# Performance work log

Measured on AMD Instinct MI355X. Metric: run time of the kernel, lower is better.

## Reference

```python
import jax, jax.numpy as jnp
import numpy as np

C_IN = 128   # pair channel dim
H = 4        # heads
DH = 32      # per-head dim (c_hidden // no_heads = 128 // 4)
R = 96       # low-rank bias rank (hard-coded self.Rank)
N = 384      # sequence length (pair rep is N x N)
S_DIM = 449  # s_inputs feature dim (c_in + 449 into bias MLPs)
MLP_H = 256  # bias MLP hidden width
EPS = 1e-5


def setup_inputs() -> dict:
    key = jax.random.key(0)
    ks = jax.random.split(key, 16)
    w = lambda k, shp, s=0.02: (jax.random.normal(k, shp) * s).astype(jnp.float32)
    return {
        "x": jax.random.normal(ks[0], (N, N, C_IN), dtype=jnp.float32),
        "s_inputs": jax.random.normal(ks[1], (N, S_DIM), dtype=jnp.float32),
        "ln_gamma": jnp.ones((C_IN,), jnp.float32),
        "ln_beta": jnp.zeros((C_IN,), jnp.float32),
        # q flashbias MLP (Linear->Tanh->Linear->Tanh->Linear, no bias)
        "Wq1": w(ks[2], (C_IN + S_DIM, MLP_H)),
        "Wq2": w(ks[3], (MLP_H, MLP_H)),
        "Wq3": w(ks[4], (MLP_H, H * R)),
        # k flashbias MLP
        "Wk1": w(ks[5], (C_IN + S_DIM, MLP_H)),
        "Wk2": w(ks[6], (MLP_H, MLP_H)),
        "Wk3": w(ks[7], (MLP_H, H * R)),
        # OpenFold-style gated Attention params
        "Wq_att": w(ks[8], (C_IN, H * DH)),
        "Wk_att": w(ks[9], (C_IN, H * DH)),
        "Wv_att": w(ks[10], (C_IN, H * DH)),
        "Wg": w(ks[11], (C_IN, H * DH)),
        "bg": jnp.zeros((H * DH,), jnp.float32),
        "Wo": w(ks[12], (H * DH, C_IN)),
        "bo": jnp.zeros((C_IN,), jnp.float32),
        "id": 10,  # id < 16 -> low-rank flashbias path
    }


def _layer_norm(x, gamma, beta):
    mu = jnp.mean(x, axis=-1, keepdims=True)
    var = jnp.var(x, axis=-1, keepdims=True)
    return (x - mu) * jax.lax.rsqrt(var + EPS) * gamma + beta


def _bias_mlp(z, W1, W2, W3):
    # [N, C+449] -> [N, H*R] -> [1, H, N, R]
    h = jnp.tanh(jnp.tanh(z @ W1) @ W2) @ W3
    return jnp.transpose(h.reshape(N, H, R), (1, 0, 2))[None]


def reference(x, s_inputs, ln_gamma, ln_beta, Wq1, Wq2, Wq3, Wk1, Wk2, Wk3,
              Wq_att, Wk_att, Wv_att, Wg, bg, Wo, bo, id=10):
    # starting=True, eval mode, s_inputs given, id < 16 -> low-rank bias path
    x = _layer_norm(x, ln_gamma, ln_beta)                       # [N, N, C]

    # low-rank triangle-bias factors (shared across rows, broadcast over dim 0)
    q_bias = _bias_mlp(jnp.concatenate([x.mean(1), s_inputs], -1), Wq1, Wq2, Wq3)  # [1,H,N,R]
    k_bias = _bias_mlp(jnp.concatenate([x.mean(0), s_inputs], -1), Wk1, Wk2, Wk3)  # [1,H,N,R]

    # multi-head attention over the last sequence axis, per row
    def heads(z, W):  # [N, N, C] -> [N, H, N, DH]
        return jnp.transpose((z @ W).reshape(N, N, H, DH), (0, 2, 1, 3))

    q = heads(x, Wq_att) * (1.0 / np.sqrt(DH)).astype(np.float32)
    k = heads(x, Wk_att)
    v = heads(x, Wv_att)

    scores = jnp.einsum("ihqd,ihkd->ihqk", q, k)                # [N,H,N,N]
    scores = scores + jnp.einsum("bhqr,bhkr->bhqk", q_bias, k_bias)  # broadcast over rows
    a = jax.nn.softmax(scores, axis=-1)

    o = jnp.einsum("ihqk,ihkd->ihqd", a, v)                     # [N,H,N,DH]
    o = jnp.transpose(o, (0, 2, 1, 3)).reshape(N, N, H * DH)
    g = jax.nn.sigmoid(x @ Wg + bg)                              # gating
    out = (g * o) @ Wo + bo                                      # [N, N, C]
    return out
```

## Files before the change

### kernel.cpp

```cpp
#include <hip/hip_runtime.h>
#include <cstdint>
#include <cstddef>

typedef _Float16 f16;
typedef __attribute__((ext_vector_type(2))) _Float16 f16x2;
typedef __attribute__((ext_vector_type(4))) _Float16 f16x4;
typedef __attribute__((ext_vector_type(8))) _Float16 f16x8;
typedef __attribute__((ext_vector_type(4))) float f32x4;

#define MFMA_16x16x32(a,b,c) __builtin_amdgcn_mfma_f32_16x16x32_f16((a),(b),(c),0,0,0)
#define MFMA_16x16x16(a,b,c) __builtin_amdgcn_mfma_f32_16x16x16f16((a),(b),(c),0,0,0)

#define NSEQ 384
#define CIN 128
#define NH 4
#define DHD 32
#define RNK 96
#define SDIM 449
#define MHID 256
#define NN (NSEQ*NSEQ)
#define LOG2E 1.4426950408889634f

#define KPAD 608
#define ZSTR 616
#define HSTR 264
#define OFF_W1 0
#define SZ_W1 (MHID*KPAD)
#define OFF_W2 (2*SZ_W1)
#define SZ_W2 (MHID*MHID)
#define OFF_W3 (OFF_W2 + 2*SZ_W2)
#define SZ_W3 ((NH*RNK)*MHID)
#define WMLP_TOT (OFF_W3 + 2*SZ_W3)

__global__ __launch_bounds__(256) void k_convert(const float* __restrict__ Wq, const float* __restrict__ Wk,
    const float* __restrict__ Wv, const float* __restrict__ Wg, const float* __restrict__ Wo,
    f16* __restrict__ W4T, f16* __restrict__ WoT) {
  int idx = blockIdx.x*256 + threadIdx.x;
  int c = idx >> 7, kk = idx & 127;
  if (c < 512) {
    int mat = c >> 7, cc = c & 127;
    const float* src = mat==0 ? Wq : (mat==1 ? Wk : (mat==2 ? Wv : Wg));
    W4T[c*CIN + kk] = (f16)src[kk*CIN + cc];
  } else {
    int cc = c - 512;
    WoT[cc*CIN + kk] = (f16)Wo[kk*CIN + cc];
  }
}

__global__ __launch_bounds__(256) void k_convert2(const float* __restrict__ Wq1, const float* __restrict__ Wq2,
    const float* __restrict__ Wq3, const float* __restrict__ Wk1, const float* __restrict__ Wk2,
    const float* __restrict__ Wk3, f16* __restrict__ wmlp) {
  int idx = blockIdx.x*256 + threadIdx.x;
  float val;
  if (idx < OFF_W2) {
    int m = idx / SZ_W1, r = idx - m*SZ_W1;
    int c = r / KPAD, kk = r - c*KPAD;
    const float* src = m ? Wk1 : Wq1;
    val = (kk < SDIM + CIN) ? src[kk*MHID + c] : 0.f;
  } else if (idx < OFF_W3) {
    int r = idx - OFF_W2;
    int m = r >> 16, rr = r & 65535;
    int c = rr >> 8, kk = rr & 255;
    const float* src = m ? Wk2 : Wq2;
    val = src[kk*MHID + c];
  } else {
    int r = idx - OFF_W3;
    int m = r / SZ_W3, rr = r - m*SZ_W3;
    int c = rr >> 8, kk = rr & 255;
    const float* src = m ? Wk3 : Wq3;
    val = src[kk*(NH*RNK) + c];
  }
  wmlp[idx] = (f16)val;
}

__global__ __launch_bounds__(256) void k_ln(const float* __restrict__ x, const float* __restrict__ gamma,
    const float* __restrict__ beta, f16* __restrict__ xn, float* __restrict__ rowm) {
  int b = blockIdx.x;
  int i = b >> 2, jbase = (b & 3) * 96;
  int t = threadIdx.x, wave = t >> 6, lane = t & 63;
  int half = lane >> 5, l31 = lane & 31;
  int c0 = l31 * 4;
  __shared__ float racc[CIN];
  if (t < CIN) racc[t] = 0.f;
  float4 g4 = *(const float4*)&gamma[c0];
  float4 b4 = *(const float4*)&beta[c0];
  float a0=0,a1=0,a2=0,a3=0;
  __syncthreads();
  for (int it = 0; it < 12; ++it) {
    int j = jbase + it*8 + wave*2 + half;
    const float4 v = *(const float4*)&x[(size_t)(i*NSEQ + j)*CIN + c0];
    float s = (v.x+v.y)+(v.z+v.w);
    float ss = (v.x*v.x+v.y*v.y)+(v.z*v.z+v.w*v.w);
#pragma unroll
    for (int off = 16; off >= 1; off >>= 1) { s += __shfl_xor(s, off); ss += __shfl_xor(ss, off); }
    float mean = s * (1.0f/CIN);
    float var = ss * (1.0f/CIN) - mean*mean;
    float rs = rsqrtf(var + 1e-5f);
    float y0 = (v.x-mean)*rs*g4.x + b4.x;
    float y1 = (v.y-mean)*rs*g4.y + b4.y;
    float y2 = (v.z-mean)*rs*g4.z + b4.z;
    float y3 = (v.w-mean)*rs*g4.w + b4.w;
    f16x4 w; w[0]=(f16)y0; w[1]=(f16)y1; w[2]=(f16)y2; w[3]=(f16)y3;
    *(f16x4*)&xn[(size_t)(i*NSEQ + j)*CIN + c0] = w;
    a0+=y0; a1+=y1; a2+=y2; a3+=y3;
  }
  atomicAdd(&racc[c0], a0); atomicAdd(&racc[c0+1], a1);
  atomicAdd(&racc[c0+2], a2); atomicAdd(&racc[c0+3], a3);
  __syncthreads();
  if (t < CIN) atomicAdd(&rowm[i*CIN + t], racc[t] * (1.0f/NSEQ));
}

__global__ __launch_bounds__(256) void k_colmean(const f16* __restrict__ xn, float* __restrict__ colm) {
  int j = blockIdx.x; int t = threadIdx.x;
  int c = t & 127, half = t >> 7;
  float acc = 0.f;
  int i0 = half*192;
#pragma unroll 4
  for (int ii = i0; ii < i0 + 192; ++ii)
    acc += (float)xn[(size_t)(ii*NSEQ + j)*CIN + c];
  __shared__ float sb[256];
  sb[t] = acc;
  __syncthreads();
  if (t < 128) colm[j*CIN + t] = (sb[t] + sb[t+128]) * (1.0f/NSEQ);
}

__global__ __launch_bounds__(256) void k_mlp2(const float* __restrict__ rowm, const float* __restrict__ colm,
    const float* __restrict__ sinp, const f16* __restrict__ wmlp,
    float* __restrict__ qbT, float* __restrict__ kbT) {
  int b = blockIdx.x;
  bool isQ = b < 12;
  int r0 = (isQ ? b : b - 12) * 32;
  const float* mean = isQ ? rowm : colm;
  const f16* W1T = wmlp + (isQ ? 0 : SZ_W1);
  const f16* W2T = wmlp + OFF_W2 + (isQ ? 0 : SZ_W2);
  const f16* W3T = wmlp + OFF_W3 + (isQ ? 0 : SZ_W3);
  float* outp = isQ ? qbT : kbT;
  int t = threadIdx.x, wave = t >> 6, lane = t & 63;
  int l15 = lane & 15, quad = lane >> 4;
  int rt = wave & 1, ch = wave >> 1;

  __shared__ __align__(16) f16 z[32*ZSTR];
  __shared__ __align__(16) f16 hbuf[2][32*HSTR];

  for (int idx = t; idx < 32*KPAD; idx += 256) {
    int row = idx / KPAD, u = idx - row*KPAD;
    float v;
    if (u < CIN) v = mean[(r0+row)*CIN + u];
    else if (u < CIN + SDIM) v = sinp[(r0+row)*SDIM + (u - CIN)];
    else v = 0.f;
    z[row*ZSTR + u] = (f16)v;
  }
  __syncthreads();

  {
    f32x4 acc[8];
#pragma unroll
    for (int c = 0; c < 8; ++c) acc[c] = (f32x4){0,0,0,0};
    for (int ks = 0; ks < 19; ++ks) {
      f16x8 af = *(const f16x8*)&z[(rt*16 + l15)*ZSTR + ks*32 + quad*8];
#pragma unroll
      for (int c = 0; c < 8; ++c) {
        f16x8 bf = *(const f16x8*)&W1T[(size_t)((ch*8 + c)*16 + l15)*KPAD + ks*32 + quad*8];
        acc[c] = MFMA_16x16x32(af, bf, acc[c]);
      }
    }
#pragma unroll
    for (int c = 0; c < 8; ++c) {
      int col = (ch*8 + c)*16 + l15;
#pragma unroll
      for (int r = 0; r < 4; ++r) {
        float th = 1.f - 2.f/(1.f + __expf(2.f*acc[c][r]));
        hbuf[0][(rt*16 + quad*4 + r)*HSTR + col] = (f16)th;
      }
    }
  }
  __syncthreads();

  {
    f32x4 acc[8];
#pragma unroll
    for (int c = 0; c < 8; ++c) acc[c] = (f32x4){0,0,0,0};
    for (int ks = 0; ks < 8; ++ks) {
      f16x8 af = *(const f16x8*)&hbuf[0][(rt*16 + l15)*HSTR + ks*32 + quad*8];
#pragma unroll
      for (int c = 0; c < 8; ++c) {
        f16x8 bf = *(const f16x8*)&W2T[(size_t)((ch*8 + c)*16 + l15)*MHID + ks*32 + quad*8];
        acc[c] = MFMA_16x16x32(af, bf, acc[c]);
      }
    }
#pragma unroll
    for (int c = 0; c < 8; ++c) {
      int col = (ch*8 + c)*16 + l15;
#pragma unroll
      for (int r = 0; r < 4; ++r) {
        float th = 1.f - 2.f/(1.f + __expf(2.f*acc[c][r]));
        hbuf[1][(rt*16 + quad*4 + r)*HSTR + col] = (f16)th;
      }
    }
  }
  __syncthreads();

  {
    f32x4 acc[12];
#pragma unroll
    for (int c = 0; c < 12; ++c) acc[c] = (f32x4){0,0,0,0};
    for (int ks = 0; ks < 8; ++ks) {
      f16x8 af = *(const f16x8*)&hbuf[1][(rt*16 + l15)*HSTR + ks*32 + quad*8];
#pragma unroll
      for (int c = 0; c < 12; ++c) {
        f16x8 bf = *(const f16x8*)&W3T[(size_t)((ch*12 + c)*16 + l15)*MHID + ks*32 + quad*8];
        acc[c] = MFMA_16x16x32(af, bf, acc[c]);
      }
    }
#pragma unroll
    for (int c = 0; c < 12; ++c) {
      int o = (ch*12 + c)*16 + l15;
#pragma unroll
      for (int r = 0; r < 4; ++r)
        outp[o*NSEQ + r0 + rt*16 + quad*4 + r] = acc[c][r];
    }
  }
}

__global__ __launch_bounds__(128) void k_bias(const float* __restrict__ qbT, const float* __restrict__ kbT,
    float* __restrict__ bias4) {
  int b = blockIdx.x;
  int h = b / 96, kg = b - h*96;
  int t = threadIdx.x;
  __shared__ float4 kr[RNK];
  if (t < RNK) kr[t] = *(const float4*)&kbT[(size_t)(h*RNK + t)*NSEQ + kg*4];
  __syncthreads();
  float acc[3][4];
#pragma unroll
  for (int m = 0; m < 3; ++m)
#pragma unroll
    for (int r = 0; r < 4; ++r) acc[m][r] = 0.f;
  for (int r = 0; r < RNK; ++r) {
    float4 kv = kr[r];
    const float* qrow = qbT + (size_t)(h*RNK + r)*NSEQ;
    float q0 = qrow[t], q1 = qrow[t+128], q2 = qrow[t+256];
    acc[0][0]+=q0*kv.x; acc[0][1]+=q0*kv.y; acc[0][2]+=q0*kv.z; acc[0][3]+=q0*kv.w;
    acc[1][0]+=q1*kv.x; acc[1][1]+=q1*kv.y; acc[1][2]+=q1*kv.z; acc[1][3]+=q1*kv.w;
    acc[2][0]+=q2*kv.x; acc[2][1]+=q2*kv.y; acc[2][2]+=q2*kv.z; acc[2][3]+=q2*kv.w;
  }
#pragma unroll
  for (int m = 0; m < 3; ++m) {
    int q = t + m*128;
    f32x4 w; w[0]=acc[m][0]*LOG2E; w[1]=acc[m][1]*LOG2E; w[2]=acc[m][2]*LOG2E; w[3]=acc[m][3]*LOG2E;
    *(f32x4*)&bias4[((size_t)b*NSEQ + q)*4] = w;
  }
}

__global__ __launch_bounds__(256) void k_proj(const f16* __restrict__ xn, const f16* __restrict__ W4T,
    const float* __restrict__ bg, f16* __restrict__ qb, f16* __restrict__ kb, f16* __restrict__ vb,
    f16* __restrict__ gb) {
  int mb = blockIdx.x;
  int t = threadIdx.x, wave = t >> 6, lane = t & 63;
  int l15 = lane & 15, quad = lane >> 4;
  int m0 = wave*32;
  __shared__ __align__(16) f16 Bs[128*128];
  size_t grow = (size_t)mb*128 + m0;
  f16x8 af[2][4];
#pragma unroll
  for (int mt = 0; mt < 2; ++mt)
#pragma unroll
    for (int kt = 0; kt < 4; ++kt)
      af[mt][kt] = *(const f16x8*)&xn[(grow + mt*16 + l15)*CIN + (kt*4 + quad)*8];
  int i = mb/3, j0 = (mb - (mb/3)*3)*128 + m0;
  for (int nb = 0; nb < 4; ++nb) {
    for (int p = 0; p < 8; ++p) {
      int c = p*256 + t; int row = c >> 4, ci = c & 15;
      int sw = (ci ^ (row & 15)) * 8;
      *(f16x8*)&Bs[row*128 + sw] = *(const f16x8*)&W4T[(size_t)(nb*128 + row)*CIN + ci*8];
    }
    __syncthreads();
#pragma unroll
    for (int ct = 0; ct < 8; ++ct) {
      f32x4 acc0 = (f32x4){0,0,0,0}, acc1 = (f32x4){0,0,0,0};
#pragma unroll
      for (int kt = 0; kt < 4; ++kt) {
        f16x8 bf = *(const f16x8*)&Bs[(ct*16 + l15)*128 + ((kt*4 + quad) ^ l15)*8];
        acc0 = MFMA_16x16x32(af[0][kt], bf, acc0);
        acc1 = MFMA_16x16x32(af[1][kt], bf, acc1);
      }
      int col = nb*128 + ct*16 + l15;
      int cc = col & 127;
      int hh = cc >> 5, d = cc & 31;
      if (nb == 3) {
        float bgv = bg[cc];
#pragma unroll
        for (int mt = 0; mt < 2; ++mt) {
          f32x4 a = mt ? acc1 : acc0;
#pragma unroll
          for (int r = 0; r < 4; ++r) {
            int jj = j0 + mt*16 + quad*4 + r;
            float sg = 1.0f/(1.0f + __expf(-(a[r] + bgv)));
            gb[(size_t)(i*NSEQ + jj)*CIN + cc] = (f16)sg;
          }
        }
      } else if (nb == 2) {
#pragma unroll
        for (int mt = 0; mt < 2; ++mt) {
          f32x4 a = mt ? acc1 : acc0;
#pragma unroll
          for (int r = 0; r < 4; ++r) {
            int jj = j0 + mt*16 + quad*4 + r;
            vb[((size_t)(i*NH + hh)*DHD + d)*NSEQ + jj] = (f16)a[r];
          }
        }
      } else {
        f16* dstb = nb==0 ? qb : kb;
        float scale = nb==0 ? 0.25503576722f : 1.0f;
#pragma unroll
        for (int mt = 0; mt < 2; ++mt) {
          f32x4 a = mt ? acc1 : acc0;
#pragma unroll
          for (int r = 0; r < 4; ++r) {
            int jj = j0 + mt*16 + quad*4 + r;
            dstb[((size_t)(i*NH + hh)*NSEQ + jj)*DHD + d] = (f16)(a[r]*scale);
          }
        }
      }
    }
    __syncthreads();
  }
}

__global__ __launch_bounds__(256, 4) void k_attn(const f16* __restrict__ qg, const f16* __restrict__ kg,
    const f16* __restrict__ vg, const float* __restrict__ bias4, f16* __restrict__ og) {
  int b = blockIdx.x; int h = b / NSEQ; int i = b - h*NSEQ;
  int t = threadIdx.x; int wave = t >> 6; int lane = t & 63;
  int l15 = lane & 15, quad = lane >> 4;
  size_t base = (size_t)(i*NH + h) * NSEQ * DHD;
  int qt0 = wave*6;
  f16x8 qf[6];
#pragma unroll
  for (int s = 0; s < 6; ++s)
    qf[s] = *(const f16x8*)&qg[base + (size_t)((qt0+s)*16 + l15)*DHD + quad*8];
  f32x4 oa[6][2];
  float lsum[6];
#pragma unroll
  for (int s = 0; s < 6; ++s) { lsum[s] = 0.f; oa[s][0] = (f32x4){0,0,0,0}; oa[s][1] = (f32x4){0,0,0,0}; }
  const f16* kp  = kg + base + (size_t)l15*DHD + quad*8;
  const f16* vt  = vg + base;
  const f16* vp0 = vt + (size_t)l15*NSEQ + quad*4;
  const f16* vp1 = vt + (size_t)(l15+16)*NSEQ + quad*4;
  const float* bp = bias4 + (((size_t)h*96 + quad)*NSEQ + qt0*16 + l15)*4;
  for (int kt = 0; kt < 24; ++kt) {
    f16x8 kf = *(const f16x8*)kp;
    f16x4 vf0 = *(const f16x4*)(vp0 + kt*16);
    f16x4 vf1 = *(const f16x4*)(vp1 + kt*16);
    f32x4 cb[6];
#pragma unroll
    for (int s = 0; s < 6; ++s) cb[s] = *(const f32x4*)(bp + s*64);
    kp += 16*DHD; bp += 4*NSEQ*4;
#pragma unroll
    for (int s = 0; s < 6; ++s) {
      f32x4 st = MFMA_16x16x32(kf, qf[s], cb[s]);
      float p0 = __builtin_amdgcn_exp2f(st[0]);
      float p1 = __builtin_amdgcn_exp2f(st[1]);
      float p2 = __builtin_amdgcn_exp2f(st[2]);
      float p3 = __builtin_amdgcn_exp2f(st[3]);
      lsum[s] += (p0 + p1) + (p2 + p3);
      f16x4 pa; pa[0]=(f16)p0; pa[1]=(f16)p1; pa[2]=(f16)p2; pa[3]=(f16)p3;
      oa[s][0] = MFMA_16x16x16(pa, vf0, oa[s][0]);
      oa[s][1] = MFMA_16x16x16(pa, vf1, oa[s][1]);
    }
  }
#pragma unroll
  for (int s = 0; s < 6; ++s) {
    float lf = lsum[s];
    lf += __shfl_xor(lf, 16);
    lf += __shfl_xor(lf, 32);
    float inv = 1.0f / lf;
#pragma unroll
    for (int r = 0; r < 4; ++r) {
      float invr = __shfl(inv, quad*4 + r);
      int qrow = (qt0+s)*16 + quad*4 + r;
      size_t ob = (size_t)(i*NSEQ + qrow)*(NH*DHD) + h*DHD;
      og[ob + l15]      = (f16)(oa[s][0][r] * invr);
      og[ob + 16 + l15] = (f16)(oa[s][1][r] * invr);
    }
  }
}

__global__ __launch_bounds__(256) void k_final(const f16* __restrict__ gb, const f16* __restrict__ ob,
    const f16* __restrict__ WoT, const float* __restrict__ bo, float* __restrict__ out) {
  int mb = blockIdx.x;
  int t = threadIdx.x, wave = t >> 6, lane = t & 63;
  int l15 = lane & 15, quad = lane >> 4;
  __shared__ __align__(16) f16 Bs[128*128];
  for (int p = 0; p < 8; ++p) {
    int c = p*256 + t; int row = c >> 4, ci = c & 15;
    int sw = (ci ^ (row & 15)) * 8;
    *(f16x8*)&Bs[row*128 + sw] = *(const f16x8*)&WoT[row*CIN + ci*8];
  }
  int m0 = wave*32;
  size_t grow = (size_t)mb*128 + m0;
  f16x8 af[2][4];
#pragma unroll
  for (int mt = 0; mt < 2; ++mt)
#pragma unroll
    for (int kt = 0; kt < 4; ++kt) {
      size_t off = (grow + mt*16 + l15)*CIN + (kt*4 + quad)*8;
      f16x8 gv = *(const f16x8*)&gb[off];
      f16x8 ov = *(const f16x8*)&ob[off];
      af[mt][kt] = gv*ov;
    }
  __syncthreads();
#pragma unroll
  for (int ct = 0; ct < 8; ++ct) {
    f32x4 acc0 = (f32x4){0,0,0,0}, acc1 = (f32x4){0,0,0,0};
#pragma unroll
    for (int kt = 0; kt < 4; ++kt) {
      f16x8 bf = *(const f16x8*)&Bs[(ct*16 + l15)*128 + ((kt*4 + quad) ^ l15)*8];
      acc0 = MFMA_16x16x32(af[0][kt], bf, acc0);
      acc1 = MFMA_16x16x32(af[1][kt], bf, acc1);
    }
    float bov = bo[ct*16 + l15];
#pragma unroll
    for (int mt = 0; mt < 2; ++mt) {
      f32x4 a = mt ? acc1 : acc0;
#pragma unroll
      for (int r = 0; r < 4; ++r) {
        int mrow = (int)(grow) + mt*16 + quad*4 + r;
        out[(size_t)mrow*CIN + ct*16 + l15] = a[r] + bov;
      }
    }
  }
}

extern "C" void kernel_launch(void* const* d_in, const int* in_sizes, int n_in,
                              void* d_out, int out_size, void* d_ws, size_t ws_size,
                              hipStream_t stream) {
  (void)in_sizes; (void)n_in; (void)out_size; (void)ws_size;
  const float* x    = (const float*)d_in[0];
  const float* sinp = (const float*)d_in[1];
  const float* gam  = (const float*)d_in[2];
  const float* bet  = (const float*)d_in[3];
  const float* Wq1  = (const float*)d_in[4];
  const float* Wq2  = (const float*)d_in[5];
  const float* Wq3  = (const float*)d_in[6];
  const float* Wk1  = (const float*)d_in[7];
  const float* Wk2  = (const float*)d_in[8];
  const float* Wk3  = (const float*)d_in[9];
  const float* Wqa  = (const float*)d_in[10];
  const float* Wka  = (const float*)d_in[11];
  const float* Wva  = (const float*)d_in[12];
  const float* Wg   = (const float*)d_in[13];
  const float* bg   = (const float*)d_in[14];
  const float* Wo   = (const float*)d_in[15];
  const float* bo   = (const float*)d_in[16];
  float* out = (float*)d_out;

  char* w = (char*)d_ws;
  auto carve = [&](size_t bytes) { char* p = w; w += (bytes + 255) & ~(size_t)255; return p; };
  f16*   xn    = (f16*)carve((size_t)NN*CIN*2);
  f16*   qb    = (f16*)carve((size_t)NN*CIN*2);
  f16*   kb    = (f16*)carve((size_t)NN*CIN*2);
  f16*   vb    = (f16*)carve((size_t)NN*CIN*2);
  f16*   gbuf  = (f16*)carve((size_t)NN*CIN*2);
  float* bias4 = (float*)carve((size_t)NH*NSEQ*NSEQ*4);
  float* rowm  = (float*)carve((size_t)NSEQ*CIN*4);
  float* colm  = (float*)carve((size_t)NSEQ*CIN*4);
  float* qbT   = (float*)carve((size_t)(NH*RNK)*NSEQ*4);
  float* kbT   = (float*)carve((size_t)(NH*RNK)*NSEQ*4);
  f16*   W4T   = (f16*)carve((size_t)512*CIN*2);
  f16*   WoT   = (f16*)carve((size_t)CIN*CIN*2);
  f16*   wmlp  = (f16*)carve((size_t)WMLP_TOT*2);
  f16*   obuf  = xn;

  hipMemsetAsync(rowm, 0, (size_t)NSEQ*CIN*4, stream);
  k_convert<<<320, 256, 0, stream>>>(Wqa, Wka, Wva, Wg, Wo, W4T, WoT);
  k_convert2<<<WMLP_TOT/256, 256, 0, stream>>>(Wq1, Wq2, Wq3, Wk1, Wk2, Wk3, wmlp);
  k_ln<<<NSEQ*4, 256, 0, stream>>>(x, gam, bet, xn, rowm);
  k_colmean<<<NSEQ, 256, 0, stream>>>(xn, colm);
  k_mlp2<<<24, 256, 0, stream>>>(rowm, colm, sinp, wmlp, qbT, kbT);
  k_bias<<<NH*96, 128, 0, stream>>>(qbT, kbT, bias4);
  k_proj<<<1152, 256, 0, stream>>>(xn, W4T, bg, qb, kb, vb, gbuf);
  k_attn<<<NH*NSEQ, 256, 0, stream>>>(qb, kb, vb, bias4, obuf);
  k_final<<<1152, 256, 0, stream>>>(gbuf, obuf, WoT, bo, out);
}
```

Before: 446.9 us.

## Fold low-rank bias into attention QK via extra MFMAs, drop bias kernel

Removes the k_bias kernel and its materialized 4xNxN fp32 bias tensor. The attention kernel instead computes the bias on the fly as extra rank-96 MFMA k-steps, using fp16 q/k bias factors written directly by the MLP kernel (LOG2E folded into the q factor). V is now stored in the same row-major layout as Q/K and gathered with strided scalar loads. Occupancy hint drops from 4 to 2 blocks per CU because of the extra register fragments. Bias precision drops from fp32 to fp16 inputs.

```diff
diff --git a/kernel.cpp b/kernel.cpp
--- a/kernel.cpp
+++ b/kernel.cpp
@@ -126,7 +126,7 @@
 
 __global__ __launch_bounds__(256) void k_mlp2(const float* __restrict__ rowm, const float* __restrict__ colm,
     const float* __restrict__ sinp, const f16* __restrict__ wmlp,
-    float* __restrict__ qbT, float* __restrict__ kbT) {
+    f16* __restrict__ qb2, f16* __restrict__ kb2) {
   int b = blockIdx.x;
   bool isQ = b < 12;
   int r0 = (isQ ? b : b - 12) * 32;
@@ -134,7 +134,8 @@
   const f16* W1T = wmlp + (isQ ? 0 : SZ_W1);
   const f16* W2T = wmlp + OFF_W2 + (isQ ? 0 : SZ_W2);
   const f16* W3T = wmlp + OFF_W3 + (isQ ? 0 : SZ_W3);
-  float* outp = isQ ? qbT : kbT;
+  f16* dst = isQ ? qb2 : kb2;
+  float oscale = isQ ? LOG2E : 1.0f;
   int t = threadIdx.x, wave = t >> 6, lane = t & 63;
   int l15 = lane & 15, quad = lane >> 4;
   int rt = wave & 1, ch = wave >> 1;
@@ -214,40 +215,15 @@
     }
 #pragma unroll
     for (int c = 0; c < 12; ++c) {
-      int o = (ch*12 + c)*16 + l15;
-#pragma unroll
-      for (int r = 0; r < 4; ++r)
-        outp[o*NSEQ + r0 + rt*16 + quad*4 + r] = acc[c][r];
-    }
-  }
-}
-
-__global__ __launch_bounds__(128) void k_bias(const float* __restrict__ qbT, const float* __restrict__ kbT,
-    float* __restrict__ bias4) {
-  int b = blockIdx.x;
-  int h = b / 96, kg = b - h*96;
-  int t = threadIdx.x;
-  __shared__ float4 kr[RNK];
-  if (t < RNK) kr[t] = *(const float4*)&kbT[(size_t)(h*RNK + t)*NSEQ + kg*4];
-  __syncthreads();
-  float acc[3][4];
-#pragma unroll
-  for (int m = 0; m < 3; ++m)
-#pragma unroll
-    for (int r = 0; r < 4; ++r) acc[m][r] = 0.f;
-  for (int r = 0; r < RNK; ++r) {
-    float4 kv = kr[r];
-    const float* qrow = qbT + (size_t)(h*RNK + r)*NSEQ;
-    float q0 = qrow[t], q1 = qrow[t+128], q2 = qrow[t+256];
-    acc[0][0]+=q0*kv.x; acc[0][1]+=q0*kv.y; acc[0][2]+=q0*kv.z; acc[0][3]+=q0*kv.w;
-    acc[1][0]+=q1*kv.x; acc[1][1]+=q1*kv.y; acc[1][2]+=q1*kv.z; acc[1][3]+=q1*kv.w;
-    acc[2][0]+=q2*kv.x; acc[2][1]+=q2*kv.y; acc[2][2]+=q2*kv.z; acc[2][3]+=q2*kv.w;
-  }
-#pragma unroll
-  for (int m = 0; m < 3; ++m) {
-    int q = t + m*128;
-    f32x4 w; w[0]=acc[m][0]*LOG2E; w[1]=acc[m][1]*LOG2E; w[2]=acc[m][2]*LOG2E; w[3]=acc[m][3]*LOG2E;
-    *(f32x4*)&bias4[((size_t)b*NSEQ + q)*4] = w;
+      int T = ch*12 + c;
+      int hh = T / 6;
+      int rr = (T - hh*6)*16 + l15;
+#pragma unroll
+      for (int r = 0; r < 4; ++r) {
+        int q = r0 + rt*16 + quad*4 + r;
+        dst[((size_t)hh*NSEQ + q)*RNK + rr] = (f16)(acc[c][r] * oscale);
+      }
+    }
   }
 }
 
@@ -298,18 +274,8 @@
             gb[(size_t)(i*NSEQ + jj)*CIN + cc] = (f16)sg;
           }
         }
-      } else if (nb == 2) {
-#pragma unroll
-        for (int mt = 0; mt < 2; ++mt) {
-          f32x4 a = mt ? acc1 : acc0;
-#pragma unroll
-          for (int r = 0; r < 4; ++r) {
-            int jj = j0 + mt*16 + quad*4 + r;
-            vb[((size_t)(i*NH + hh)*DHD + d)*NSEQ + jj] = (f16)a[r];
-          }
-        }
       } else {
-        f16* dstb = nb==0 ? qb : kb;
+        f16* dstb = nb==0 ? qb : (nb==1 ? kb : vb);
         float scale = nb==0 ? 0.25503576722f : 1.0f;
 #pragma unroll
         for (int mt = 0; mt < 2; ++mt) {
@@ -326,37 +292,47 @@
   }
 }
 
-__global__ __launch_bounds__(256, 4) void k_attn(const f16* __restrict__ qg, const f16* __restrict__ kg,
-    const f16* __restrict__ vg, const float* __restrict__ bias4, f16* __restrict__ og) {
+__global__ __launch_bounds__(256, 2) void k_attn(const f16* __restrict__ qg, const f16* __restrict__ kg,
+    const f16* __restrict__ vg, const f16* __restrict__ qb2, const f16* __restrict__ kb2,
+    f16* __restrict__ og) {
   int b = blockIdx.x; int h = b / NSEQ; int i = b - h*NSEQ;
   int t = threadIdx.x; int wave = t >> 6; int lane = t & 63;
   int l15 = lane & 15, quad = lane >> 4;
   size_t base = (size_t)(i*NH + h) * NSEQ * DHD;
+  size_t hb = (size_t)h * NSEQ * RNK;
   int qt0 = wave*6;
-  f16x8 qf[6];
-#pragma unroll
-  for (int s = 0; s < 6; ++s)
-    qf[s] = *(const f16x8*)&qg[base + (size_t)((qt0+s)*16 + l15)*DHD + quad*8];
+  f16x8 qf[6][4];
+#pragma unroll
+  for (int s = 0; s < 6; ++s) {
+    int qrow = (qt0+s)*16 + l15;
+    qf[s][0] = *(const f16x8*)&qg[base + (size_t)qrow*DHD + quad*8];
+    qf[s][1] = *(const f16x8*)&qb2[hb + (size_t)qrow*RNK + quad*8];
+    qf[s][2] = *(const f16x8*)&qb2[hb + (size_t)qrow*RNK + 32 + quad*8];
+    qf[s][3] = *(const f16x8*)&qb2[hb + (size_t)qrow*RNK + 64 + quad*8];
+  }
   f32x4 oa[6][2];
   float lsum[6];
 #pragma unroll
   for (int s = 0; s < 6; ++s) { lsum[s] = 0.f; oa[s][0] = (f32x4){0,0,0,0}; oa[s][1] = (f32x4){0,0,0,0}; }
   const f16* kp  = kg + base + (size_t)l15*DHD + quad*8;
-  const f16* vt  = vg + base;
-  const f16* vp0 = vt + (size_t)l15*NSEQ + quad*4;
-  const f16* vp1 = vt + (size_t)(l15+16)*NSEQ + quad*4;
-  const float* bp = bias4 + (((size_t)h*96 + quad)*NSEQ + qt0*16 + l15)*4;
+  const f16* kbp = kb2 + hb + (size_t)l15*RNK + quad*8;
+  const f16* vp  = vg + base + (size_t)(quad*4)*DHD + l15;
+  const f32x4 zero = (f32x4){0,0,0,0};
   for (int kt = 0; kt < 24; ++kt) {
-    f16x8 kf = *(const f16x8*)kp;
-    f16x4 vf0 = *(const f16x4*)(vp0 + kt*16);
-    f16x4 vf1 = *(const f16x4*)(vp1 + kt*16);
-    f32x4 cb[6];
-#pragma unroll
-    for (int s = 0; s < 6; ++s) cb[s] = *(const f32x4*)(bp + s*64);
-    kp += 16*DHD; bp += 4*NSEQ*4;
+    f16x8 kf0 = *(const f16x8*)kp;
+    f16x8 kf1 = *(const f16x8*)(kbp);
+    f16x8 kf2 = *(const f16x8*)(kbp + 32);
+    f16x8 kf3 = *(const f16x8*)(kbp + 64);
+    f16x4 vf0, vf1;
+#pragma unroll
+    for (int jj = 0; jj < 4; ++jj) { vf0[jj] = vp[jj*DHD]; vf1[jj] = vp[jj*DHD + 16]; }
+    kp += 16*DHD; kbp += 16*RNK; vp += 16*DHD;
 #pragma unroll
     for (int s = 0; s < 6; ++s) {
-      f32x4 st = MFMA_16x16x32(kf, qf[s], cb[s]);
+      f32x4 st = MFMA_16x16x32(kf0, qf[s][0], zero);
+      st = MFMA_16x16x32(kf1, qf[s][1], st);
+      st = MFMA_16x16x32(kf2, qf[s][2], st);
+      st = MFMA_16x16x32(kf3, qf[s][3], st);
       float p0 = __builtin_amdgcn_exp2f(st[0]);
       float p1 = __builtin_amdgcn_exp2f(st[1]);
       float p2 = __builtin_amdgcn_exp2f(st[2]);
@@ -460,11 +436,10 @@
   f16*   kb    = (f16*)carve((size_t)NN*CIN*2);
   f16*   vb    = (f16*)carve((size_t)NN*CIN*2);
   f16*   gbuf  = (f16*)carve((size_t)NN*CIN*2);
-  float* bias4 = (float*)carve((size_t)NH*NSEQ*NSEQ*4);
   float* rowm  = (float*)carve((size_t)NSEQ*CIN*4);
   float* colm  = (float*)carve((size_t)NSEQ*CIN*4);
-  float* qbT   = (float*)carve((size_t)(NH*RNK)*NSEQ*4);
-  float* kbT   = (float*)carve((size_t)(NH*RNK)*NSEQ*4);
+  f16*   qb2   = (f16*)carve((size_t)NH*NSEQ*RNK*2);
+  f16*   kb2   = (f16*)carve((size_t)NH*NSEQ*RNK*2);
   f16*   W4T   = (f16*)carve((size_t)512*CIN*2);
   f16*   WoT   = (f16*)carve((size_t)CIN*CIN*2);
   f16*   wmlp  = (f16*)carve((size_t)WMLP_TOT*2);
@@ -475,9 +450,8 @@
   k_convert2<<<WMLP_TOT/256, 256, 0, stream>>>(Wq1, Wq2, Wq3, Wk1, Wk2, Wk3, wmlp);
   k_ln<<<NSEQ*4, 256, 0, stream>>>(x, gam, bet, xn, rowm);
   k_colmean<<<NSEQ, 256, 0, stream>>>(xn, colm);
-  k_mlp2<<<24, 256, 0, stream>>>(rowm, colm, sinp, wmlp, qbT, kbT);
-  k_bias<<<NH*96, 128, 0, stream>>>(qbT, kbT, bias4);
+  k_mlp2<<<24, 256, 0, stream>>>(rowm, colm, sinp, wmlp, qb2, kb2);
   k_proj<<<1152, 256, 0, stream>>>(xn, W4T, bg, qb, kb, vb, gbuf);
-  k_attn<<<NH*NSEQ, 256, 0, stream>>>(qb, kb, vb, bias4, obuf);
+  k_attn<<<NH*NSEQ, 256, 0, stream>>>(qb, kb, vb, qb2, kb2, obuf);
   k_final<<<1152, 256, 0, stream>>>(gbuf, obuf, WoT, bo, out);
 }
```

Result: no change. 453.8 us (+1.5%).
